# Kernel tuning notes

Measured on AMD Instinct MI355X. Metric: run time of the kernel, lower is better.

## Reference

```python
import jax, jax.numpy as jnp
import numpy as np

B, T, D, H, K = 2, 1024, 1024, 4096, 8


def setup_inputs() -> dict:
    key = jax.random.key(0)
    ks = jax.random.split(key, 5)
    x = jax.random.normal(ks[0], (B, T, D), dtype=jnp.float32)
    # hard one-hot routing weights per token (no learned router)
    expert_ids = jax.random.randint(ks[1], (B, T), 0, K)
    combine_weights = jax.nn.one_hot(expert_ids, K, dtype=jnp.float32)
    scale_in = 1.0 / np.sqrt(D)
    scale_h = 1.0 / np.sqrt(H)
    wg = jax.random.normal(ks[2], (K, D, H), dtype=jnp.float32) * scale_in
    wu = jax.random.normal(ks[3], (K, D, H), dtype=jnp.float32) * scale_in
    wd = jax.random.normal(ks[4], (K, H, D), dtype=jnp.float32) * scale_h
    return {"x": x, "combine_weights": combine_weights, "wg": wg, "wu": wu, "wd": wd}


def reference(x, combine_weights, wg, wu, wd):
    # Each expert is a SwiGLU FFN: down( silu(gate(x)) * up(x) ).
    # Dense baseline: every token runs through all K experts (as in source).
    g = jnp.einsum('btd,kdh->btkh', x, wg)          # [B,T,K,H]
    u = jnp.einsum('btd,kdh->btkh', x, wu)          # [B,T,K,H]
    h = jax.nn.silu(g) * u                          # [B,T,K,H]
    expert_outs = jnp.einsum('btkh,khd->btkd', h, wd)  # [B,T,K,D]
    y = jnp.einsum('btk,btkd->btd', combine_weights, expert_outs)
    return y.astype(x.dtype)
```

## Files before the change

### kernel.cpp

```cpp
#include <hip/hip_runtime.h>

typedef __attribute__((ext_vector_type(8))) short bf16x8;
typedef __attribute__((ext_vector_type(4))) float f32x4;
typedef unsigned short u16;

#define NTOK 2048
#define DDIM 1024
#define HDIM 4096
#define KEXP 8

#define BM 320
#define BN 128
#define BK 64
#define LDSS 72
#define NDESC 16

__device__ __forceinline__ u16 f2bf(float f) {
  union { float f; unsigned int u; } c; c.f = f;
  unsigned int u = c.u;
  return (u16)((u + 0x7FFFu + ((u >> 16) & 1u)) >> 16);
}
__device__ __forceinline__ unsigned pk2(float a, float b) {
  return (unsigned)f2bf(a) | ((unsigned)f2bf(b) << 16);
}

__global__ void route_kernel(const float* __restrict__ cw, int* __restrict__ offs,
                             int* __restrict__ perm, float* __restrict__ wsel,
                             int* __restrict__ desc) {
  __shared__ int cnt[KEXP];
  __shared__ int base[KEXP];
  const int t = threadIdx.x;
  if (t < KEXP) cnt[t] = 0;
  __syncthreads();
  int eid[8]; float wv[8];
  #pragma unroll
  for (int i = 0; i < 8; i++) {
    const int tok = t * 8 + i;
    const float* p = cw + tok * KEXP;
    int best = 0; float bw = p[0];
    #pragma unroll
    for (int k = 1; k < KEXP; k++) { float v = p[k]; if (v > bw) { bw = v; best = k; } }
    eid[i] = best; wv[i] = bw;
    atomicAdd(&cnt[best], 1);
  }
  __syncthreads();
  if (t == 0) {
    int s = 0, nd = 0;
    for (int k = 0; k < KEXP; k++) {
      const int ck = cnt[k];
      base[k] = s; offs[k] = s;
      for (int m0 = 0; m0 < ck && nd < NDESC; m0 += BM)
        desc[nd++] = (k << 12) | (s + m0);
      s += ck;
    }
    offs[KEXP] = s;
    for (; nd < NDESC; nd++) desc[nd] = -1;
  }
  __syncthreads();
  #pragma unroll
  for (int i = 0; i < 8; i++) {
    const int tok = t * 8 + i;
    const int pos = atomicAdd(&base[eid[i]], 1);
    perm[pos] = tok;
    wsel[pos] = wv[i];
  }
}

__global__ void gather_x(const float* __restrict__ x, const int* __restrict__ perm,
                         u16* __restrict__ Xb) {
  const int slot = blockIdx.x;
  const int tok = perm[slot];
  const int t = threadIdx.x;
  float4 v = ((const float4*)(x + (size_t)tok * DDIM))[t];
  ushort4 o; o.x = f2bf(v.x); o.y = f2bf(v.y); o.z = f2bf(v.z); o.w = f2bf(v.w);
  ((ushort4*)(Xb + (size_t)slot * DDIM))[t] = o;
}

__global__ __launch_bounds__(1024, 4) void gemm_swiglu(
    const u16* __restrict__ Xb,
    const float* __restrict__ wg, const float* __restrict__ wu,
    const int* __restrict__ offs, const int* __restrict__ desc,
    u16* __restrict__ Hb) {
  __shared__ u16 As[BM * LDSS];
  __shared__ u16 Bg[BN * LDSS];
  __shared__ u16 Bu[BN * LDSS];

  const int d = desc[blockIdx.y];
  if (d < 0) return;
  const int e = d >> 12;
  const int slot0 = d & 0xFFF;
  const int Msub = offs[e + 1] - slot0;
  const int n0 = blockIdx.x * BN;

  const int t = threadIdx.x;
  const int lane = t & 63;
  const int W = t >> 6;
  const int wm = W >> 2;
  const int wn = W & 3;
  const int l15 = lane & 15;
  const int lhi = lane >> 4;

  const bool do_a = t < 640;
  const int a_row = t >> 1;
  const int a_ck = (t & 1) * 32;
  const u16* a_src = Xb + (size_t)min(slot0 + a_row, NTOK - 1) * DDIM + a_ck;
  u16* a_dst = As + a_row * LDSS + a_ck;

  const int tb = t & 511;
  const float* Wsrc = ((t < 512) ? wg : wu) + (size_t)e * DDIM * HDIM;
  const int b_n2 = (tb & 63) * 2;
  const int b_kk = (tb >> 6) * 8;
  const float* b_src = Wsrc + (size_t)b_kk * HDIM + n0 + b_n2;
  u16* b_dst = ((t < 512) ? Bg : Bu) + b_n2 * LDSS + b_kk;

  float2 br[8];
  f32x4 accg[5][2] = {};
  f32x4 accu[5][2] = {};

  #pragma unroll
  for (int i = 0; i < 8; i++) br[i] = *(const float2*)(b_src + (size_t)i * HDIM);

  #pragma unroll 1
  for (int it = 0; it < DDIM / BK; ++it) {
    const int k0 = it * BK;
    if (it) __syncthreads();
    if (do_a) {
      const uint4* s = (const uint4*)(a_src + k0);
      uint4 s0 = s[0], s1 = s[1], s2 = s[2], s3 = s[3];
      uint4* dd = (uint4*)a_dst;
      dd[0] = s0; dd[1] = s1; dd[2] = s2; dd[3] = s3;
    }
    {
      uint4 w0, w1;
      w0.x = pk2(br[0].x, br[1].x); w0.y = pk2(br[2].x, br[3].x);
      w0.z = pk2(br[4].x, br[5].x); w0.w = pk2(br[6].x, br[7].x);
      w1.x = pk2(br[0].y, br[1].y); w1.y = pk2(br[2].y, br[3].y);
      w1.z = pk2(br[4].y, br[5].y); w1.w = pk2(br[6].y, br[7].y);
      *(uint4*)b_dst = w0;
      *(uint4*)(b_dst + LDSS) = w1;
    }
    if (it + 1 < DDIM / BK) {
      const float* bs = b_src + (size_t)(k0 + BK) * HDIM;
      #pragma unroll
      for (int i = 0; i < 8; i++) br[i] = *(const float2*)(bs + (size_t)i * HDIM);
    }
    asm volatile("s_waitcnt lgkmcnt(0)" ::: "memory");
    __builtin_amdgcn_sched_barrier(0);
    __builtin_amdgcn_s_barrier();
    __builtin_amdgcn_sched_barrier(0);
    #pragma unroll
    for (int ks = 0; ks < 2; ks++) {
      const int kof = ks * 32 + lhi * 8;
      bf16x8 bgf[2], buf[2];
      #pragma unroll
      for (int fn = 0; fn < 2; fn++) {
        bgf[fn] = *(const bf16x8*)(Bg + (wn * 32 + fn * 16 + l15) * LDSS + kof);
        buf[fn] = *(const bf16x8*)(Bu + (wn * 32 + fn * 16 + l15) * LDSS + kof);
      }
      #pragma unroll
      for (int fm = 0; fm < 5; fm++) {
        bf16x8 af = *(const bf16x8*)(As + (wm * 80 + fm * 16 + l15) * LDSS + kof);
        #pragma unroll
        for (int fn = 0; fn < 2; fn++) {
          accg[fm][fn] = __builtin_amdgcn_mfma_f32_16x16x32_bf16(af, bgf[fn], accg[fm][fn], 0, 0, 0);
          accu[fm][fn] = __builtin_amdgcn_mfma_f32_16x16x32_bf16(af, buf[fn], accu[fm][fn], 0, 0, 0);
        }
      }
    }
  }

  #pragma unroll
  for (int fm = 0; fm < 5; fm++) {
    #pragma unroll
    for (int i = 0; i < 4; i++) {
      const int row = wm * 80 + fm * 16 + lhi * 4 + i;
      if (row < Msub) {
        const size_t base = (size_t)(slot0 + row) * HDIM + n0 + wn * 32;
        #pragma unroll
        for (int fn = 0; fn < 2; fn++) {
          const float g = accg[fm][fn][i];
          const float u = accu[fm][fn][i];
          const float h = (g / (1.0f + __expf(-g))) * u;
          Hb[base + fn * 16 + l15] = f2bf(h);
        }
      }
    }
  }
}

__global__ __launch_bounds__(1024, 4) void gemm_down(
    const u16* __restrict__ Hb, const float* __restrict__ wd,
    const int* __restrict__ offs, const int* __restrict__ desc,
    const int* __restrict__ perm, const float* __restrict__ wsel,
    float* __restrict__ y) {
  __shared__ u16 As[BM * LDSS];
  __shared__ u16 Bs[BN * LDSS];

  const int d = desc[blockIdx.y];
  if (d < 0) return;
  const int e = d >> 12;
  const int slot0 = d & 0xFFF;
  const int Msub = offs[e + 1] - slot0;
  const int n0 = blockIdx.x * BN;
  const int kbase = blockIdx.z * (HDIM / 4);

  const float* Wd = wd + (size_t)e * HDIM * DDIM;

  const int t = threadIdx.x;
  const int lane = t & 63;
  const int W = t >> 6;
  const int wm = W >> 2;
  const int wn = W & 3;
  const int l15 = lane & 15;
  const int lhi = lane >> 4;

  const bool do_a = t < 640;
  const int a_row = t >> 1;
  const int a_ck = (t & 1) * 32;
  const u16* a_src = Hb + (size_t)min(slot0 + a_row, NTOK - 1) * HDIM + kbase + a_ck;
  u16* a_dst = As + a_row * LDSS + a_ck;

  const int b_n2 = (t & 63) * 2;
  const int b_kk = (t >> 6) * 4;
  const float* b_src = Wd + (size_t)(kbase + b_kk) * DDIM + n0 + b_n2;
  u16* b_dst = Bs + b_n2 * LDSS + b_kk;

  float2 br[4];
  f32x4 acc[5][2] = {};

  #pragma unroll
  for (int i = 0; i < 4; i++) br[i] = *(const float2*)(b_src + (size_t)i * DDIM);

  const int NIT = (HDIM / 4) / BK;
  #pragma unroll 1
  for (int it = 0; it < NIT; ++it) {
    const int k0 = it * BK;
    if (it) __syncthreads();
    if (do_a) {
      const uint4* s = (const uint4*)(a_src + k0);
      uint4 s0 = s[0], s1 = s[1], s2 = s[2], s3 = s[3];
      uint4* dd = (uint4*)a_dst;
      dd[0] = s0; dd[1] = s1; dd[2] = s2; dd[3] = s3;
    }
    {
      uint2 w0, w1;
      w0.x = pk2(br[0].x, br[1].x); w0.y = pk2(br[2].x, br[3].x);
      w1.x = pk2(br[0].y, br[1].y); w1.y = pk2(br[2].y, br[3].y);
      *(uint2*)b_dst = w0;
      *(uint2*)(b_dst + LDSS) = w1;
    }
    if (it + 1 < NIT) {
      const float* bs = b_src + (size_t)(k0 + BK) * DDIM;
      #pragma unroll
      for (int i = 0; i < 4; i++) br[i] = *(const float2*)(bs + (size_t)i * DDIM);
    }
    asm volatile("s_waitcnt lgkmcnt(0)" ::: "memory");
    __builtin_amdgcn_sched_barrier(0);
    __builtin_amdgcn_s_barrier();
    __builtin_amdgcn_sched_barrier(0);
    #pragma unroll
    for (int ks = 0; ks < 2; ks++) {
      const int kof = ks * 32 + lhi * 8;
      bf16x8 bf[2];
      #pragma unroll
      for (int fn = 0; fn < 2; fn++)
        bf[fn] = *(const bf16x8*)(Bs + (wn * 32 + fn * 16 + l15) * LDSS + kof);
      #pragma unroll
      for (int fm = 0; fm < 5; fm++) {
        bf16x8 af = *(const bf16x8*)(As + (wm * 80 + fm * 16 + l15) * LDSS + kof);
        #pragma unroll
        for (int fn = 0; fn < 2; fn++)
          acc[fm][fn] = __builtin_amdgcn_mfma_f32_16x16x32_bf16(af, bf[fn], acc[fm][fn], 0, 0, 0);
      }
    }
  }

  #pragma unroll
  for (int fm = 0; fm < 5; fm++) {
    #pragma unroll
    for (int i = 0; i < 4; i++) {
      const int row = wm * 80 + fm * 16 + lhi * 4 + i;
      if (row < Msub) {
        const int slot = slot0 + row;
        const int tok = perm[slot];
        const float w = wsel[slot];
        const size_t base = (size_t)tok * DDIM + n0 + wn * 32;
        #pragma unroll
        for (int fn = 0; fn < 2; fn++)
          atomicAdd(y + base + fn * 16 + l15, acc[fm][fn][i] * w);
      }
    }
  }
}

extern "C" void kernel_launch(void* const* d_in, const int* in_sizes, int n_in,
                              void* d_out, int out_size, void* d_ws, size_t ws_size,
                              hipStream_t stream) {
  const float* x  = (const float*)d_in[0];
  const float* cw = (const float*)d_in[1];
  const float* wg = (const float*)d_in[2];
  const float* wu = (const float*)d_in[3];
  const float* wd = (const float*)d_in[4];
  float* y = (float*)d_out;

  char* ws = (char*)d_ws;
  int* offs   = (int*)ws;
  int* desc   = (int*)(ws + 64);
  int* perm   = (int*)(ws + 128);
  float* wsel = (float*)(ws + 128 + NTOK * 4);
  u16* Xb = (u16*)(ws + 32768);
  u16* Hb = (u16*)(ws + 32768 + (size_t)NTOK * DDIM * 2);

  hipMemsetAsync(d_out, 0, (size_t)NTOK * DDIM * sizeof(float), stream);
  route_kernel<<<1, 256, 0, stream>>>(cw, offs, perm, wsel, desc);
  gather_x<<<NTOK, 256, 0, stream>>>(x, perm, Xb);
  gemm_swiglu<<<dim3(HDIM / BN, NDESC), 1024, 0, stream>>>(Xb, wg, wu, offs, desc, Hb);
  gemm_down<<<dim3(DDIM / BN, NDESC, 4), 1024, 0, stream>>>(Hb, wd, offs, desc, perm, wsel, y);
}
```

Before: 164.0 us.

## Shrink GEMM N-tiles and split gate/up across waves with LDS exchange

Both grouped GEMMs move from 1024-thread blocks with BN=128 to 512-thread blocks with narrower N tiles: 32 columns in the gate/up kernel and 64 in the down kernel. This gives many more blocks and less LDS per block. In the SwiGLU kernel, half the waves compute the gate product and half the up product. The up accumulators are then passed through LDS so the gate waves can apply SiLU and the multiply. The goal is more blocks in flight and lower register pressure. The cost is that the A tile is reloaded for every narrower N tile, giving more global and LDS traffic, plus an extra LDS exchange with barriers at the end.

```diff
diff --git a/kernel.cpp b/kernel.cpp
--- a/kernel.cpp
+++ b/kernel.cpp
@@ -10,7 +10,6 @@
 #define KEXP 8
 
 #define BM 320
-#define BN 128
 #define BK 64
 #define LDSS 72
 #define NDESC 16
@@ -76,132 +75,150 @@
   ((ushort4*)(Xb + (size_t)slot * DDIM))[t] = o;
 }
 
-__global__ __launch_bounds__(1024, 4) void gemm_swiglu(
+__global__ __launch_bounds__(512, 4) void gemm_swiglu(
     const u16* __restrict__ Xb,
     const float* __restrict__ wg, const float* __restrict__ wu,
     const int* __restrict__ offs, const int* __restrict__ desc,
     u16* __restrict__ Hb) {
   __shared__ u16 As[BM * LDSS];
-  __shared__ u16 Bg[BN * LDSS];
-  __shared__ u16 Bu[BN * LDSS];
+  __shared__ u16 Bg[32 * LDSS];
+  __shared__ u16 Bu[32 * LDSS];
 
   const int d = desc[blockIdx.y];
   if (d < 0) return;
   const int e = d >> 12;
   const int slot0 = d & 0xFFF;
   const int Msub = offs[e + 1] - slot0;
-  const int n0 = blockIdx.x * BN;
+  const int n0 = blockIdx.x * 32;
 
   const int t = threadIdx.x;
   const int lane = t & 63;
   const int W = t >> 6;
-  const int wm = W >> 2;
-  const int wn = W & 3;
+  const int wm = W & 3;
+  const bool isU = W >= 4;
   const int l15 = lane & 15;
   const int lhi = lane >> 4;
 
-  const bool do_a = t < 640;
-  const int a_row = t >> 1;
+  const int a_row1 = t >> 1;
   const int a_ck = (t & 1) * 32;
-  const u16* a_src = Xb + (size_t)min(slot0 + a_row, NTOK - 1) * DDIM + a_ck;
-  u16* a_dst = As + a_row * LDSS + a_ck;
-
-  const int tb = t & 511;
-  const float* Wsrc = ((t < 512) ? wg : wu) + (size_t)e * DDIM * HDIM;
-  const int b_n2 = (tb & 63) * 2;
-  const int b_kk = (tb >> 6) * 8;
-  const float* b_src = Wsrc + (size_t)b_kk * HDIM + n0 + b_n2;
-  u16* b_dst = ((t < 512) ? Bg : Bu) + b_n2 * LDSS + b_kk;
-
-  float2 br[8];
-  f32x4 accg[5][2] = {};
-  f32x4 accu[5][2] = {};
-
-  #pragma unroll
-  for (int i = 0; i < 8; i++) br[i] = *(const float2*)(b_src + (size_t)i * HDIM);
+  const u16* a_src1 = Xb + (size_t)min(slot0 + a_row1, NTOK - 1) * DDIM + a_ck;
+  u16* a_dst1 = As + a_row1 * LDSS + a_ck;
+  const bool do_a2 = t < 128;
+  const u16* a_src2 = Xb + (size_t)min(slot0 + a_row1 + 256, NTOK - 1) * DDIM + a_ck;
+  u16* a_dst2 = As + (a_row1 + 256) * LDSS + a_ck;
+
+  const int tb = t & 255;
+  const float* Wsrc = ((t < 256) ? wg : wu) + (size_t)e * DDIM * HDIM;
+  const int b_n = tb & 31;
+  const int b_kk = (tb >> 5) * 8;
+  const float* b_src = Wsrc + (size_t)b_kk * HDIM + n0 + b_n;
+  u16* b_dst = ((t < 256) ? Bg : Bu) + b_n * LDSS + b_kk;
+
+  float br[8];
+  f32x4 acc[5][2] = {};
+
+  #pragma unroll
+  for (int i = 0; i < 8; i++) br[i] = b_src[(size_t)i * HDIM];
 
   #pragma unroll 1
   for (int it = 0; it < DDIM / BK; ++it) {
     const int k0 = it * BK;
     if (it) __syncthreads();
-    if (do_a) {
-      const uint4* s = (const uint4*)(a_src + k0);
+    {
+      const uint4* s = (const uint4*)(a_src1 + k0);
       uint4 s0 = s[0], s1 = s[1], s2 = s[2], s3 = s[3];
-      uint4* dd = (uint4*)a_dst;
+      uint4* dd = (uint4*)a_dst1;
       dd[0] = s0; dd[1] = s1; dd[2] = s2; dd[3] = s3;
+      if (do_a2) {
+        const uint4* q = (const uint4*)(a_src2 + k0);
+        uint4 q0 = q[0], q1 = q[1], q2 = q[2], q3 = q[3];
+        uint4* d2 = (uint4*)a_dst2;
+        d2[0] = q0; d2[1] = q1; d2[2] = q2; d2[3] = q3;
+      }
     }
     {
-      uint4 w0, w1;
-      w0.x = pk2(br[0].x, br[1].x); w0.y = pk2(br[2].x, br[3].x);
-      w0.z = pk2(br[4].x, br[5].x); w0.w = pk2(br[6].x, br[7].x);
-      w1.x = pk2(br[0].y, br[1].y); w1.y = pk2(br[2].y, br[3].y);
-      w1.z = pk2(br[4].y, br[5].y); w1.w = pk2(br[6].y, br[7].y);
-      *(uint4*)b_dst = w0;
-      *(uint4*)(b_dst + LDSS) = w1;
+      uint4 w;
+      w.x = pk2(br[0], br[1]); w.y = pk2(br[2], br[3]);
+      w.z = pk2(br[4], br[5]); w.w = pk2(br[6], br[7]);
+      *(uint4*)b_dst = w;
     }
     if (it + 1 < DDIM / BK) {
       const float* bs = b_src + (size_t)(k0 + BK) * HDIM;
       #pragma unroll
-      for (int i = 0; i < 8; i++) br[i] = *(const float2*)(bs + (size_t)i * HDIM);
+      for (int i = 0; i < 8; i++) br[i] = bs[(size_t)i * HDIM];
     }
     asm volatile("s_waitcnt lgkmcnt(0)" ::: "memory");
     __builtin_amdgcn_sched_barrier(0);
     __builtin_amdgcn_s_barrier();
     __builtin_amdgcn_sched_barrier(0);
+    const u16* Bmat = isU ? Bu : Bg;
     #pragma unroll
     for (int ks = 0; ks < 2; ks++) {
       const int kof = ks * 32 + lhi * 8;
-      bf16x8 bgf[2], buf[2];
-      #pragma unroll
-      for (int fn = 0; fn < 2; fn++) {
-        bgf[fn] = *(const bf16x8*)(Bg + (wn * 32 + fn * 16 + l15) * LDSS + kof);
-        buf[fn] = *(const bf16x8*)(Bu + (wn * 32 + fn * 16 + l15) * LDSS + kof);
-      }
+      bf16x8 bf[2];
+      #pragma unroll
+      for (int fn = 0; fn < 2; fn++)
+        bf[fn] = *(const bf16x8*)(Bmat + (fn * 16 + l15) * LDSS + kof);
       #pragma unroll
       for (int fm = 0; fm < 5; fm++) {
         bf16x8 af = *(const bf16x8*)(As + (wm * 80 + fm * 16 + l15) * LDSS + kof);
         #pragma unroll
-        for (int fn = 0; fn < 2; fn++) {
-          accg[fm][fn] = __builtin_amdgcn_mfma_f32_16x16x32_bf16(af, bgf[fn], accg[fm][fn], 0, 0, 0);
-          accu[fm][fn] = __builtin_amdgcn_mfma_f32_16x16x32_bf16(af, buf[fn], accu[fm][fn], 0, 0, 0);
+        for (int fn = 0; fn < 2; fn++)
+          acc[fm][fn] = __builtin_amdgcn_mfma_f32_16x16x32_bf16(af, bf[fn], acc[fm][fn], 0, 0, 0);
+      }
+    }
+  }
+
+  float* Ubuf = (float*)As;
+  __syncthreads();
+  if (isU) {
+    #pragma unroll
+    for (int fm = 0; fm < 5; fm++) {
+      #pragma unroll
+      for (int i = 0; i < 4; i++) {
+        const int row = wm * 80 + fm * 16 + lhi * 4 + i;
+        #pragma unroll
+        for (int fn = 0; fn < 2; fn++)
+          Ubuf[row * 33 + fn * 16 + l15] = acc[fm][fn][i];
+      }
+    }
+  }
+  __syncthreads();
+  if (!isU) {
+    #pragma unroll
+    for (int fm = 0; fm < 5; fm++) {
+      #pragma unroll
+      for (int i = 0; i < 4; i++) {
+        const int row = wm * 80 + fm * 16 + lhi * 4 + i;
+        if (row < Msub) {
+          const size_t base = (size_t)(slot0 + row) * HDIM + n0;
+          #pragma unroll
+          for (int fn = 0; fn < 2; fn++) {
+            const float g = acc[fm][fn][i];
+            const float u = Ubuf[row * 33 + fn * 16 + l15];
+            const float h = (g / (1.0f + __expf(-g))) * u;
+            Hb[base + fn * 16 + l15] = f2bf(h);
+          }
         }
       }
     }
   }
-
-  #pragma unroll
-  for (int fm = 0; fm < 5; fm++) {
-    #pragma unroll
-    for (int i = 0; i < 4; i++) {
-      const int row = wm * 80 + fm * 16 + lhi * 4 + i;
-      if (row < Msub) {
-        const size_t base = (size_t)(slot0 + row) * HDIM + n0 + wn * 32;
-        #pragma unroll
-        for (int fn = 0; fn < 2; fn++) {
-          const float g = accg[fm][fn][i];
-          const float u = accu[fm][fn][i];
-          const float h = (g / (1.0f + __expf(-g))) * u;
-          Hb[base + fn * 16 + l15] = f2bf(h);
-        }
-      }
-    }
-  }
-}
-
-__global__ __launch_bounds__(1024, 4) void gemm_down(
+}
+
+__global__ __launch_bounds__(512, 4) void gemm_down(
     const u16* __restrict__ Hb, const float* __restrict__ wd,
     const int* __restrict__ offs, const int* __restrict__ desc,
     const int* __restrict__ perm, const float* __restrict__ wsel,
     float* __restrict__ y) {
   __shared__ u16 As[BM * LDSS];
-  __shared__ u16 Bs[BN * LDSS];
+  __shared__ u16 Bs[64 * LDSS];
 
   const int d = desc[blockIdx.y];
   if (d < 0) return;
   const int e = d >> 12;
   const int slot0 = d & 0xFFF;
   const int Msub = offs[e + 1] - slot0;
-  const int n0 = blockIdx.x * BN;
+  const int n0 = blockIdx.x * 64;
   const int kbase = blockIdx.z * (HDIM / 4);
 
   const float* Wd = wd + (size_t)e * HDIM * DDIM;
@@ -209,19 +226,21 @@
   const int t = threadIdx.x;
   const int lane = t & 63;
   const int W = t >> 6;
-  const int wm = W >> 2;
-  const int wn = W & 3;
+  const int wm = W >> 1;
+  const int wn = W & 1;
   const int l15 = lane & 15;
   const int lhi = lane >> 4;
 
-  const bool do_a = t < 640;
-  const int a_row = t >> 1;
+  const int a_row1 = t >> 1;
   const int a_ck = (t & 1) * 32;
-  const u16* a_src = Hb + (size_t)min(slot0 + a_row, NTOK - 1) * HDIM + kbase + a_ck;
-  u16* a_dst = As + a_row * LDSS + a_ck;
-
-  const int b_n2 = (t & 63) * 2;
-  const int b_kk = (t >> 6) * 4;
+  const u16* a_src1 = Hb + (size_t)min(slot0 + a_row1, NTOK - 1) * HDIM + kbase + a_ck;
+  u16* a_dst1 = As + a_row1 * LDSS + a_ck;
+  const bool do_a2 = t < 128;
+  const u16* a_src2 = Hb + (size_t)min(slot0 + a_row1 + 256, NTOK - 1) * HDIM + kbase + a_ck;
+  u16* a_dst2 = As + (a_row1 + 256) * LDSS + a_ck;
+
+  const int b_n2 = (t & 31) * 2;
+  const int b_kk = (t >> 5) * 4;
   const float* b_src = Wd + (size_t)(kbase + b_kk) * DDIM + n0 + b_n2;
   u16* b_dst = Bs + b_n2 * LDSS + b_kk;
 
@@ -236,11 +255,17 @@
   for (int it = 0; it < NIT; ++it) {
     const int k0 = it * BK;
     if (it) __syncthreads();
-    if (do_a) {
-      const uint4* s = (const uint4*)(a_src + k0);
+    {
+      const uint4* s = (const uint4*)(a_src1 + k0);
       uint4 s0 = s[0], s1 = s[1], s2 = s[2], s3 = s[3];
-      uint4* dd = (uint4*)a_dst;
+      uint4* dd = (uint4*)a_dst1;
       dd[0] = s0; dd[1] = s1; dd[2] = s2; dd[3] = s3;
+      if (do_a2) {
+        const uint4* q = (const uint4*)(a_src2 + k0);
+        uint4 q0 = q[0], q1 = q[1], q2 = q[2], q3 = q[3];
+        uint4* d2 = (uint4*)a_dst2;
+        d2[0] = q0; d2[1] = q1; d2[2] = q2; d2[3] = q3;
+      }
     }
     {
       uint2 w0, w1;
@@ -314,6 +339,6 @@
   hipMemsetAsync(d_out, 0, (size_t)NTOK * DDIM * sizeof(float), stream);
   route_kernel<<<1, 256, 0, stream>>>(cw, offs, perm, wsel, desc);
   gather_x<<<NTOK, 256, 0, stream>>>(x, perm, Xb);
-  gemm_swiglu<<<dim3(HDIM / BN, NDESC), 1024, 0, stream>>>(Xb, wg, wu, offs, desc, Hb);
-  gemm_down<<<dim3(DDIM / BN, NDESC, 4), 1024, 0, stream>>>(Hb, wd, offs, desc, perm, wsel, y);
-}
+  gemm_swiglu<<<dim3(HDIM / 32, NDESC), 512, 0, stream>>>(Xb, wg, wu, offs, desc, Hb);
+  gemm_down<<<dim3(DDIM / 64, NDESC, 4), 512, 0, stream>>>(Hb, wd, offs, desc, perm, wsel, y);
+}
```

After: 189.2 us. 1.15x slower.
